# Kernel optimization log

Measured on AMD Instinct MI355X. Metric: run time of the kernel, lower is better.

## Reference

```python
import jax, jax.numpy as jnp
from jax import lax
import numpy as np

DN = ('NHWC', 'HWIO', 'NHWC')  # NHWC activations, HWIO kernels (TF layout)
EPS = 1e-3


def setup_inputs() -> dict:
    key = jax.random.key(0)
    ks = jax.random.split(key, 6)
    B, H, W, C = 16, 64, 64, 256
    x = jax.random.normal(ks[0], (B, H, W, C), jnp.float32)
    # per-sample predicted kernels (scaled to keep activations well-conditioned)
    depthwise_kernels = jax.random.normal(ks[1], (B, 3, 3, C, C), jnp.float32) * 0.02
    pointwise_kernels = jax.random.normal(ks[2], (B, 1, 1, C, C), jnp.float32) * 0.06
    biases = jax.random.normal(ks[3], (B, C), jnp.float32) * 0.1
    # shared trailing Conv2D layer params
    conv_w = jax.random.normal(ks[4], (3, 3, C, C), jnp.float32) * 0.02
    conv_b = jnp.zeros((C,), jnp.float32)
    return dict(x=x, depthwise_kernels=depthwise_kernels,
                pointwise_kernels=pointwise_kernels, biases=biases,
                conv_w=conv_w, conv_b=conv_b)


def _instance_norm(x):
    # tf.nn.moments over spatial dims (population variance), eps=0.001
    mean = jnp.mean(x, axis=(1, 2), keepdims=True)
    var = jnp.var(x, axis=(1, 2), keepdims=True)
    return (x - mean) * lax.rsqrt(var + EPS)


def _reflect_pad_hw(x, p=1):
    pad = [(0, 0)] * (x.ndim - 3) + [(p, p), (p, p), (0, 0)]
    return jnp.pad(x, pad, mode='reflect')


def _per_sample_conv(xi, dk, pk, bi):
    # xi: [H,W,C]; dk: [3,3,C,Cm]; pk: [1,1,Cm,Co]; bi: [Co]
    xp = _reflect_pad_hw(xi)[None]  # [1,H+2,W+2,C]
    y = lax.conv_general_dilated(xp, dk, (1, 1), 'VALID', dimension_numbers=DN)
    y = lax.conv_general_dilated(y, pk, (1, 1), 'VALID', dimension_numbers=DN)
    return (y + bi)[0]


def reference(x, depthwise_kernels, pointwise_kernels, biases, conv_w, conv_b):
    x = _instance_norm(x)
    # per-sample kernels -> vmap over batch (replaces tf.map_fn)
    x = jax.vmap(_per_sample_conv)(x, depthwise_kernels, pointwise_kernels, biases)
    # shared Conv2D: reflect pad + VALID conv + bias
    xp = _reflect_pad_hw(x)
    y = lax.conv_general_dilated(xp, conv_w, (1, 1), 'VALID', dimension_numbers=DN)
    return y + conv_b
```

## Files before the change

kernel.cpp:

```cpp
#include <hip/hip_runtime.h>


typedef __bf16 bf16x8 __attribute__((ext_vector_type(8)));
typedef float f32x4 __attribute__((ext_vector_type(4)));

__device__ __forceinline__ float bf2f(unsigned short v) {
    return __uint_as_float(((unsigned int)v) << 16);
}
__device__ __forceinline__ unsigned short f2bf(float f) {
    unsigned int u = __float_as_uint(f);
    unsigned int r = (u + 0x7FFFu + ((u >> 16) & 1u)) >> 16;
    return (unsigned short)r;
}
__device__ __forceinline__ float ldg_elem(const void* p, size_t idx, bool isbf) {
    return isbf ? bf2f(((const unsigned short*)p)[idx]) : ((const float*)p)[idx];
}

__device__ __forceinline__ void gload16(const void* g, void* l) {
    __builtin_amdgcn_global_load_lds(
        (__attribute__((address_space(1))) void*)(unsigned long long)g,
        (__attribute__((address_space(3))) void*)(unsigned long long)l,
        16, 0, 0);
}

#define RAW_BARRIER() do { asm volatile("" ::: "memory"); \
                           __builtin_amdgcn_s_barrier();   \
                           asm volatile("" ::: "memory"); } while (0)

__global__ void detect_dtype(const unsigned short* __restrict__ x, int* __restrict__ flag) {
    __shared__ int wild;
    if (threadIdx.x == 0) wild = 0;
    __syncthreads();
    int cnt = 0;
    for (int i = 0; i < 16; ++i) {
        float a = fabsf(bf2f(x[threadIdx.x * 16 + i]));
        if (!(a < 64.f) || (a != 0.f && a < 1e-5f)) cnt++;
    }
    atomicAdd(&wild, cnt);
    __syncthreads();
    if (threadIdx.x == 0) *flag = (wild > 512) ? 0 : 1;
}

__global__ void norm_partial2(const void* __restrict__ x, const int* __restrict__ flag,
                              float* __restrict__ partS, float* __restrict__ partQ) {
    const bool isbf = (*flag != 0);
    const int b = blockIdx.x, ch = blockIdx.y;
    const int t = threadIdx.x;
    const int l = t & 63;
    const int c4 = l * 4;
    const int sp0 = t >> 6;
    const size_t base = ((size_t)(b * 4096 + ch * 128 + sp0)) * 256 + c4;
    float s[4] = {0.f, 0.f, 0.f, 0.f}, q[4] = {0.f, 0.f, 0.f, 0.f};
    if (isbf) {
        for (int i = 0; i < 32; ++i) {
            const unsigned short* p = (const unsigned short*)x + base + (size_t)i * 1024;
            ushort4 v = *(const ushort4*)p;
            float a[4] = {bf2f(v.x), bf2f(v.y), bf2f(v.z), bf2f(v.w)};
#pragma unroll
            for (int j = 0; j < 4; ++j) { s[j] += a[j]; q[j] += a[j] * a[j]; }
        }
    } else {
        for (int i = 0; i < 32; ++i) {
            float4 v = *(const float4*)((const float*)x + base + (size_t)i * 1024);
            float a[4] = {v.x, v.y, v.z, v.w};
#pragma unroll
            for (int j = 0; j < 4; ++j) { s[j] += a[j]; q[j] += a[j] * a[j]; }
        }
    }
    __shared__ float red[4][64][9];
#pragma unroll
    for (int j = 0; j < 4; ++j) { red[sp0][l][j] = s[j]; red[sp0][l][4 + j] = q[j]; }
    __syncthreads();
    if (t < 64) {
#pragma unroll
        for (int j = 0; j < 4; ++j) {
            float ss = red[0][t][j] + red[1][t][j] + red[2][t][j] + red[3][t][j];
            float qq = red[0][t][4 + j] + red[1][t][4 + j] + red[2][t][4 + j] + red[3][t][4 + j];
            int c = t * 4 + j;
            partS[(b * 32 + ch) * 256 + c] = ss;
            partQ[(b * 32 + ch) * 256 + c] = qq;
        }
    }
}

__global__ void norm_finalize2(const float* __restrict__ partS, const float* __restrict__ partQ,
                               float* __restrict__ mean, float* __restrict__ rstd) {
    const int b = blockIdx.x, c = threadIdx.x;
    float s = 0.f, q = 0.f;
    for (int k = 0; k < 32; ++k) {
        s += partS[(b * 32 + k) * 256 + c];
        q += partQ[(b * 32 + k) * 256 + c];
    }
    float m = s * (1.f / 4096.f);
    float v = q * (1.f / 4096.f) - m * m;
    mean[b * 256 + c] = m;
    rstd[b * 256 + c] = rsqrtf(v + 1e-3f);
}

__global__ void norm_apply(const void* __restrict__ x, const int* __restrict__ flag,
                           const float* __restrict__ mean, const float* __restrict__ rstd,
                           unsigned short* __restrict__ xn) {
    const bool isbf = (*flag != 0);
    size_t e = ((size_t)blockIdx.x * 256 + threadIdx.x) * 8;
    int c0 = (int)(e & 255);
    int bc = (int)(e >> 20) * 256 + c0;
    float v[8];
    if (isbf) {
        uint4 raw = *(const uint4*)((const unsigned short*)x + e);
        unsigned int rr[4] = {raw.x, raw.y, raw.z, raw.w};
#pragma unroll
        for (int i = 0; i < 4; ++i) {
            v[2 * i]     = bf2f((unsigned short)(rr[i] & 0xFFFF));
            v[2 * i + 1] = bf2f((unsigned short)(rr[i] >> 16));
        }
    } else {
        float4 f0 = *(const float4*)((const float*)x + e);
        float4 f1 = *(const float4*)((const float*)x + e + 4);
        v[0] = f0.x; v[1] = f0.y; v[2] = f0.z; v[3] = f0.w;
        v[4] = f1.x; v[5] = f1.y; v[6] = f1.z; v[7] = f1.w;
    }
    unsigned int o[4];
#pragma unroll
    for (int i = 0; i < 4; ++i) {
        unsigned short lo = f2bf((v[2 * i]     - mean[bc + 2 * i])     * rstd[bc + 2 * i]);
        unsigned short hi = f2bf((v[2 * i + 1] - mean[bc + 2 * i + 1]) * rstd[bc + 2 * i + 1]);
        o[i] = (unsigned int)lo | ((unsigned int)hi << 16);
    }
    uint4 out; out.x = o[0]; out.y = o[1]; out.z = o[2]; out.w = o[3];
    *(uint4*)(xn + e) = out;
}

template <bool SCALE>
__global__ void transpose_wk(const void* __restrict__ src, const int* __restrict__ flag,
                             unsigned short* __restrict__ dst,
                             int s_per, long dstBStride, int coStride,
                             const float* __restrict__ rstd) {
    __shared__ unsigned short tile[64][66];
    const bool isbf = (*flag != 0);
    const int sl = blockIdx.x;
    const int b = sl / s_per;
    const size_t dbase = (size_t)b * (size_t)dstBStride + (size_t)(sl % s_per) * 256;
    const int ci0 = blockIdx.y * 64, co0 = blockIdx.z * 64;
    const int t = threadIdx.x;
    const int co4 = (t & 15) * 4;
    const int r0 = t >> 4;
#pragma unroll
    for (int i = 0; i < 4; ++i) {
        int r = r0 + i * 16;
        size_t sidx = (size_t)sl * 65536 + (size_t)(ci0 + r) * 256 + co0 + co4;
        if (isbf) {
            ushort4 v = *(const ushort4*)((const unsigned short*)src + sidx);
            tile[r][co4] = v.x; tile[r][co4 + 1] = v.y;
            tile[r][co4 + 2] = v.z; tile[r][co4 + 3] = v.w;
        } else {
            float4 v = *(const float4*)((const float*)src + sidx);
            tile[r][co4] = f2bf(v.x); tile[r][co4 + 1] = f2bf(v.y);
            tile[r][co4 + 2] = f2bf(v.z); tile[r][co4 + 3] = f2bf(v.w);
        }
    }
    __syncthreads();
    const int cip = (t & 31) * 2;
    const int cob = t >> 5;
    float s0 = 1.f, s1 = 1.f;
    if (SCALE) { s0 = rstd[b * 256 + ci0 + cip]; s1 = rstd[b * 256 + ci0 + cip + 1]; }
#pragma unroll
    for (int i = 0; i < 8; ++i) {
        int co = cob + i * 8;
        unsigned short lo = tile[cip][co], hi = tile[cip + 1][co];
        if (SCALE) { lo = f2bf(bf2f(lo) * s0); hi = f2bf(bf2f(hi) * s1); }
        *(unsigned int*)(dst + dbase + (size_t)(co0 + co) * coStride + ci0 + cip) =
            (unsigned int)lo | ((unsigned int)hi << 16);
    }
}

__global__ void corr_kernel(const unsigned short* __restrict__ dkT,
                            const float* __restrict__ mean,
                            float* __restrict__ negcorr) {
    const int b = blockIdx.x;
    const int lane = threadIdx.x & 63;
    const int co = blockIdx.y * 4 + (threadIdx.x >> 6);
    const unsigned short* wp = dkT + (size_t)(b * 256 + co) * 2304;
    const float* mb = mean + b * 256;
    const int ci0 = (lane & 31) * 8;
    float4 ma = *(const float4*)(mb + ci0);
    float4 mc = *(const float4*)(mb + ci0 + 4);
    float mm[8] = {ma.x, ma.y, ma.z, ma.w, mc.x, mc.y, mc.z, mc.w};
    float sum = 0.f;
#pragma unroll
    for (int c = 0; c < 5; ++c) {
        int k = c * 512 + lane * 8;
        if (k < 2304) {
            uint4 w = *(const uint4*)(wp + k);
            unsigned int wsv[4] = {w.x, w.y, w.z, w.w};
#pragma unroll
            for (int j = 0; j < 4; ++j) {
                sum += bf2f((unsigned short)(wsv[j] & 0xFFFF)) * mm[2 * j];
                sum += bf2f((unsigned short)(wsv[j] >> 16)) * mm[2 * j + 1];
            }
        }
    }
#pragma unroll
    for (int off = 32; off > 0; off >>= 1) sum += __shfl_down(sum, off);
    if (lane == 0) negcorr[b * 256 + co] = -sum;
}

template <bool PER_SAMPLE_W, int BIAS_MODE, bool OUT_F32>
__global__ __launch_bounds__(512, 2) void conv3x3_256(const unsigned short* __restrict__ src,
                                                      const int* __restrict__ flag,
                                                      const unsigned short* __restrict__ wT,
                                                      const void* __restrict__ bias,
                                                      void* __restrict__ dst) {
    constexpr int KTOT = 2304;
    extern __shared__ unsigned short smem[];

    const int t = threadIdx.x;
    const int lane = t & 63;
    const int wave = t >> 6;
    const int wr = wave >> 2;
    const int wc = wave & 3;
    const int bid = blockIdx.x + 16 * blockIdx.z;
    const int b  = (bid & 7) + ((bid >> 3) & 1) * 8;
    const int mt = bid >> 4;
    const int m0 = mt * 256;
    const int R0 = mt * 4;
    const unsigned short* srcB = src + (size_t)b * (4096 * 256);
    const unsigned short* wB = wT + (PER_SAMPLE_W ? (size_t)b * 256 * KTOT : (size_t)0);
    const bool in_bf = (BIAS_MODE >= 2) ? (*flag != 0) : true;

    const int wx = t >> 3;
    const int wg = ((t & 7) ^ (wx & 7)) << 3;
    int wrow[6];
#pragma unroll
    for (int u = 0; u < 6; ++u) {
        int r = R0 - 1 + u;
        wrow[u] = (r < 0) ? 1 : (r > 63 ? 62 : r);
    }
    const unsigned short* winsrc[6];
#pragma unroll
    for (int u = 0; u < 6; ++u)
        winsrc[u] = srcB + ((size_t)wrow[u] * 64 + wx) * 256 + wg;
    const unsigned short* bsrc = wB + (size_t)wx * KTOT + wg;

    f32x4 acc[8][4];
#pragma unroll
    for (int i = 0; i < 8; ++i)
#pragma unroll
        for (int j = 0; j < 4; ++j) acc[i][j] = (f32x4){0.f, 0.f, 0.f, 0.f};

    const int fr = lane & 15;
    const int quad = lane >> 4;
    const int fsw = fr & 7;
    const int ksb0 = (quad ^ fsw) << 3;
    const int ksb1 = ((quad + 4) ^ fsw) << 3;
    const int rm = wr * 128;
    const int cn = wc * 64;

#pragma unroll
    for (int u = 0; u < 6; ++u)
        gload16(winsrc[u], smem + u * 4096 + wave * 512);
#pragma unroll
    for (int u = 0; u < 4; ++u)
        gload16(bsrc + (size_t)u * 64 * KTOT, smem + 49152 + u * 4096 + wave * 512);

    bf16x8 af[4][2], bfr[4][2];

    for (int cg = 0; cg < 4; ++cg) {
        const unsigned short* winb = smem + (cg & 1) * 24576;
        for (int s = 0; s < 9; ++s) {
            const int j = cg * 9 + s;
            const int dh = s / 3 - 1;
            const int dw = s % 3 - 1;

            if (s == 6 || s == 7)      asm volatile("s_waitcnt vmcnt(2)" ::: "memory");
            else if (s == 8)           asm volatile("s_waitcnt vmcnt(1)" ::: "memory");
            else                       asm volatile("s_waitcnt vmcnt(0)" ::: "memory");
            RAW_BARRIER();

            if (j < 35) {
                const int s1 = (s == 8) ? 0 : s + 1;
                const int cg1 = (s == 8) ? cg + 1 : cg;
                const int koff1 = s1 * 256 + cg1 * 64;
                unsigned short* bdst = smem + 49152 + ((j + 1) & 1) * 16384 + wave * 512;
#pragma unroll
                for (int u = 0; u < 4; ++u)
                    gload16(bsrc + (size_t)u * 64 * KTOT + koff1, bdst + u * 4096);
            }
            if (cg < 3) {
                unsigned short* wdst = smem + ((cg + 1) & 1) * 24576 + wave * 512;
                const int cgo = (cg + 1) * 64;
                if (s == 5) {
                    gload16(winsrc[0] + cgo, wdst);
                    gload16(winsrc[1] + cgo, wdst + 4096);
                } else if (s == 6) {
                    gload16(winsrc[2] + cgo, wdst + 2 * 4096);
                    gload16(winsrc[3] + cgo, wdst + 3 * 4096);
                } else if (s == 7) {
                    gload16(winsrc[4] + cgo, wdst + 4 * 4096);
                } else if (s == 8) {
                    gload16(winsrc[5] + cgo, wdst + 5 * 4096);
                }
            }

            int aoo[4][2];
#pragma unroll
            for (int mi = 0; mi < 4; ++mi) {
                int ww = mi * 16 + fr + dw;
                ww = (ww < 0) ? 1 : (ww > 63 ? 62 : ww);
                const int x7 = ww & 7;
                aoo[mi][0] = ww * 64 + ((quad ^ x7) << 3);
                aoo[mi][1] = ww * 64 + (((quad + 4) ^ x7) << 3);
            }
            const unsigned short* A1 = winb + (wr * 2 + 1 + dh) * 4096;
            const unsigned short* A2 = A1 + 4096;
            const unsigned short* Bb = smem + 49152 + (j & 1) * 16384;

#pragma unroll
            for (int mi = 0; mi < 4; ++mi) {
                af[mi][0] = *(const bf16x8*)(A1 + aoo[mi][0]);
                af[mi][1] = *(const bf16x8*)(A1 + aoo[mi][1]);
            }
#pragma unroll
            for (int n = 0; n < 2; ++n) {
                const unsigned short* rp = Bb + (cn + n * 16 + fr) * 64;
                bfr[n][0] = *(const bf16x8*)(rp + ksb0);
                bfr[n][1] = *(const bf16x8*)(rp + ksb1);
            }
            __builtin_amdgcn_s_setprio(1);
#pragma unroll
            for (int mi = 0; mi < 4; ++mi)
#pragma unroll
                for (int n = 0; n < 2; ++n) {
                    acc[mi][n] = __builtin_amdgcn_mfma_f32_16x16x32_bf16(af[mi][0], bfr[n][0], acc[mi][n], 0, 0, 0);
                    acc[mi][n] = __builtin_amdgcn_mfma_f32_16x16x32_bf16(af[mi][1], bfr[n][1], acc[mi][n], 0, 0, 0);
                }
            __builtin_amdgcn_s_setprio(0);

#pragma unroll
            for (int n = 2; n < 4; ++n) {
                const unsigned short* rp = Bb + (cn + n * 16 + fr) * 64;
                bfr[n][0] = *(const bf16x8*)(rp + ksb0);
                bfr[n][1] = *(const bf16x8*)(rp + ksb1);
            }
            __builtin_amdgcn_s_setprio(1);
#pragma unroll
            for (int mi = 0; mi < 4; ++mi)
#pragma unroll
                for (int n = 2; n < 4; ++n) {
                    acc[mi][n] = __builtin_amdgcn_mfma_f32_16x16x32_bf16(af[mi][0], bfr[n][0], acc[mi][n], 0, 0, 0);
                    acc[mi][n] = __builtin_amdgcn_mfma_f32_16x16x32_bf16(af[mi][1], bfr[n][1], acc[mi][n], 0, 0, 0);
                }
            __builtin_amdgcn_s_setprio(0);

#pragma unroll
            for (int mi = 0; mi < 4; ++mi) {
                af[mi][0] = *(const bf16x8*)(A2 + aoo[mi][0]);
                af[mi][1] = *(const bf16x8*)(A2 + aoo[mi][1]);
            }
            __builtin_amdgcn_s_setprio(1);
#pragma unroll
            for (int mi = 0; mi < 4; ++mi)
#pragma unroll
                for (int n = 0; n < 4; ++n) {
                    acc[4 + mi][n] = __builtin_amdgcn_mfma_f32_16x16x32_bf16(af[mi][0], bfr[n][0], acc[4 + mi][n], 0, 0, 0);
                    acc[4 + mi][n] = __builtin_amdgcn_mfma_f32_16x16x32_bf16(af[mi][1], bfr[n][1], acc[4 + mi][n], 0, 0, 0);
                }
            __builtin_amdgcn_s_setprio(0);
        }
    }

    const int rbase = quad * 4;
    float bv[4];
#pragma unroll
    for (int n = 0; n < 4; ++n) {
        int nn = cn + n * 16 + fr;
        if (BIAS_MODE == 2)      bv[n] = ldg_elem(bias, b * 256 + nn, in_bf);
        else if (BIAS_MODE == 3) bv[n] = ldg_elem(bias, nn, in_bf);
        else                     bv[n] = 0.f;
    }
#pragma unroll
    for (int m = 0; m < 8; ++m) {
#pragma unroll
        for (int rr = 0; rr < 4; ++rr) {
            int mm = m0 + rm + m * 16 + rbase + rr;
            size_t rowoff = ((size_t)b * 4096 + mm) * 256;
#pragma unroll
            for (int n = 0; n < 4; ++n) {
                int nn = cn + n * 16 + fr;
                float val = acc[m][n][rr] + bv[n];
                if (OUT_F32) ((float*)dst)[rowoff + nn] = val;
                else         ((unsigned short*)dst)[rowoff + nn] = f2bf(val);
            }
        }
    }
}

template <int KSLICES, bool PER_SAMPLE_W, int BIAS_MODE, bool IS3X3, bool OUT_F32>
__global__ __launch_bounds__(512, 2) void gemm_conv_256(const unsigned short* __restrict__ src,
                                                        const int* __restrict__ flag,
                                                        const unsigned short* __restrict__ wT,
                                                        const void* __restrict__ bias,
                                                        void* __restrict__ dst) {
    constexpr int KTOT = KSLICES * 256;
    constexpr int NKT = KTOT / 64;
    static_assert(NKT >= 2, "pipeline needs >=2 K-tiles");
    extern __shared__ unsigned short smem[];

    const int t = threadIdx.x;
    const int lane = t & 63;
    const int wave = t >> 6;
    const int wr = wave >> 2;
    const int wc = wave & 3;
    const int bid = blockIdx.x + 16 * blockIdx.z;
    const int b  = (bid & 7) + ((bid >> 3) & 1) * 8;
    const int m0 = (bid >> 4) * 256;
    const unsigned short* srcB = src + (size_t)b * (4096 * 256);
    const unsigned short* wB = wT + (PER_SAMPLE_W ? (size_t)b * 256 * KTOT : (size_t)0);
    const bool in_bf = (BIAS_MODE >= 2) ? (*flag != 0) : true;

    const int trow = t >> 3;
    const int tswz = ((t & 7) ^ (trow & 7)) << 3;
    int hU[4], wU[4];
#pragma unroll
    for (int u = 0; u < 4; ++u) {
        int m = m0 + u * 64 + trow;
        hU[u] = m >> 6; wU[u] = m & 63;
    }
    const unsigned short* gBu[4];
#pragma unroll
    for (int u = 0; u < 4; ++u)
        gBu[u] = wB + (size_t)(u * 64 + trow) * KTOT + tswz;

    f32x4 acc[8][4];
#pragma unroll
    for (int i = 0; i < 8; ++i)
#pragma unroll
        for (int j = 0; j < 4; ++j) acc[i][j] = (f32x4){0.f, 0.f, 0.f, 0.f};

    const int fr = lane & 15;
    const int quad = lane >> 4;
    const int fsw = fr & 7;
    const int ks0 = ((quad) ^ fsw) << 3;
    const int ks1 = ((quad + 4) ^ fsw) << 3;
    const int rm = wr * 128;
    const int cn = wc * 64;

#pragma unroll
    for (int kt = 0; kt < 2; ++kt) {
        const int pdh = IS3X3 ? -1 : 0;
        const int pdw = IS3X3 ? -1 : 0;
        const int pchb = (kt & 3) << 6;
        unsigned short* ldsAW = smem + kt * 32768 + wave * 512;
#pragma unroll
        for (int u = 0; u < 4; ++u) {
            int hh = hU[u] + pdh; hh = (hh < 0) ? 1 : (hh > 63 ? 62 : hh);
            int ww = wU[u] + pdw; ww = (ww < 0) ? 1 : (ww > 63 ? 62 : ww);
            gload16(srcB + (size_t)((hh << 6) + ww) * 256 + pchb + tswz, ldsAW + u * 4096);
        }
#pragma unroll
        for (int u = 0; u < 4; ++u)
            gload16(gBu[u] + (size_t)kt * 64, ldsAW + 16384 + u * 4096);
    }
    asm volatile("s_waitcnt vmcnt(8)" ::: "memory");
    RAW_BARRIER();

    bf16x8 af[4][2], bfr[4][2];
    size_t aoff[4];
    int cur_s = -1;

    for (int i = 0; i < NKT; ++i) {
        const int buf = i & 1;
        const unsigned short* As_b = smem + buf * 32768;
        const unsigned short* Bs_b = As_b + 16384;
        unsigned short* ldsAW = smem + buf * 32768 + wave * 512;
        const int kt2 = i + 2;
        const bool st = (kt2 < NKT);

#pragma unroll
        for (int m = 0; m < 4; ++m) {
            const unsigned short* rp = As_b + (rm + m * 16 + fr) * 64;
            af[m][0] = *(const bf16x8*)(rp + ks0);
            af[m][1] = *(const bf16x8*)(rp + ks1);
        }
#pragma unroll
        for (int n = 0; n < 2; ++n) {
            const unsigned short* rp = Bs_b + (cn + n * 16 + fr) * 64;
            bfr[n][0] = *(const bf16x8*)(rp + ks0);
            bfr[n][1] = *(const bf16x8*)(rp + ks1);
        }
        __builtin_amdgcn_s_setprio(1);
#pragma unroll
        for (int m = 0; m < 4; ++m)
#pragma unroll
            for (int n = 0; n < 2; ++n) {
                acc[m][n] = __builtin_amdgcn_mfma_f32_16x16x32_bf16(af[m][0], bfr[n][0], acc[m][n], 0, 0, 0);
                acc[m][n] = __builtin_amdgcn_mfma_f32_16x16x32_bf16(af[m][1], bfr[n][1], acc[m][n], 0, 0, 0);
            }
        __builtin_amdgcn_s_setprio(0);

#pragma unroll
        for (int n = 2; n < 4; ++n) {
            const unsigned short* rp = Bs_b + (cn + n * 16 + fr) * 64;
            bfr[n][0] = *(const bf16x8*)(rp + ks0);
            bfr[n][1] = *(const bf16x8*)(rp + ks1);
        }
        __builtin_amdgcn_s_setprio(1);
#pragma unroll
        for (int m = 0; m < 4; ++m)
#pragma unroll
            for (int n = 2; n < 4; ++n) {
                acc[m][n] = __builtin_amdgcn_mfma_f32_16x16x32_bf16(af[m][0], bfr[n][0], acc[m][n], 0, 0, 0);
                acc[m][n] = __builtin_amdgcn_mfma_f32_16x16x32_bf16(af[m][1], bfr[n][1], acc[m][n], 0, 0, 0);
            }
        __builtin_amdgcn_s_setprio(0);

#pragma unroll
        for (int m = 0; m < 4; ++m) {
            const unsigned short* rp = As_b + (rm + 64 + m * 16 + fr) * 64;
            af[m][0] = *(const bf16x8*)(rp + ks0);
            af[m][1] = *(const bf16x8*)(rp + ks1);
        }
        __builtin_amdgcn_s_setprio(1);
#pragma unroll
        for (int m = 0; m < 4; ++m)
#pragma unroll
            for (int n = 0; n < 4; ++n) {
                acc[4 + m][n] = __builtin_amdgcn_mfma_f32_16x16x32_bf16(af[m][0], bfr[n][0], acc[4 + m][n], 0, 0, 0);
                acc[4 + m][n] = __builtin_amdgcn_mfma_f32_16x16x32_bf16(af[m][1], bfr[n][1], acc[4 + m][n], 0, 0, 0);
            }
        __builtin_amdgcn_s_setprio(0);

        RAW_BARRIER();
        if (st) {
            if (IS3X3) {
                const int s2 = kt2 >> 2;
                if (s2 != cur_s) {
                    cur_s = s2;
                    const int dh2 = s2 / 3 - 1, dw2 = s2 % 3 - 1;
#pragma unroll
                    for (int u = 0; u < 4; ++u) {
                        int hh = hU[u] + dh2; hh = (hh < 0) ? 1 : (hh > 63 ? 62 : hh);
                        int ww = wU[u] + dw2; ww = (ww < 0) ? 1 : (ww > 63 ? 62 : ww);
                        aoff[u] = (size_t)((hh << 6) + ww) * 256 + tswz;
                    }
                }
            } else if (cur_s < 0) {
                cur_s = 0;
#pragma unroll
                for (int u = 0; u < 4; ++u)
                    aoff[u] = (size_t)((hU[u] << 6) + wU[u]) * 256 + tswz;
            }
            const int chb2 = (kt2 & 3) << 6;
#pragma unroll
            for (int u = 0; u < 4; ++u)
                gload16(srcB + aoff[u] + chb2, ldsAW + u * 4096);
#pragma unroll
            for (int u = 0; u < 4; ++u)
                gload16(gBu[u] + (size_t)kt2 * 64, ldsAW + 16384 + u * 4096);
            asm volatile("s_waitcnt vmcnt(8)" ::: "memory");
        } else if (i + 1 < NKT) {
            asm volatile("s_waitcnt vmcnt(0)" ::: "memory");
        }
        RAW_BARRIER();
    }

    const int rbase = quad * 4;
    float bv[4];
#pragma unroll
    for (int n = 0; n < 4; ++n) {
        int nn = cn + n * 16 + fr;
        if (BIAS_MODE == 2)      bv[n] = ldg_elem(bias, b * 256 + nn, in_bf);
        else if (BIAS_MODE == 3) bv[n] = ldg_elem(bias, nn, in_bf);
        else                     bv[n] = 0.f;
    }
#pragma unroll
    for (int m = 0; m < 8; ++m) {
#pragma unroll
        for (int rr = 0; rr < 4; ++rr) {
            int mm = m0 + rm + m * 16 + rbase + rr;
            size_t rowoff = ((size_t)b * 4096 + mm) * 256;
#pragma unroll
            for (int n = 0; n < 4; ++n) {
                int nn = cn + n * 16 + fr;
                float val = acc[m][n][rr] + bv[n];
                if (OUT_F32) ((float*)dst)[rowoff + nn] = val;
                else         ((unsigned short*)dst)[rowoff + nn] = f2bf(val);
            }
        }
    }
}

template <int KSLICES, bool PER_SAMPLE_W, int BIAS_MODE, bool IS3X3, bool SRC_ADAPT, bool OUT_F32>
__global__ __launch_bounds__(256) void gemm_conv(const void* __restrict__ src,
                                                 const int* __restrict__ flag,
                                                 const unsigned short* __restrict__ wT,
                                                 const void* __restrict__ bias,
                                                 void* __restrict__ dst) {
    constexpr int KTOT = KSLICES * 256;
    __shared__ unsigned short As[128][40];
    __shared__ unsigned short Bs[128][40];

    const bool in_bf = (SRC_ADAPT || BIAS_MODE >= 2) ? (*flag != 0) : true;
    const int t = threadIdx.x;
    const int b = blockIdx.z;
    const int m0 = blockIdx.x * 128;
    const int n0 = blockIdx.y * 128;
    const size_t srcOfs = (size_t)b * (4096 * 256);
    const unsigned short* wB = wT + (PER_SAMPLE_W ? (size_t)b * 256 * KTOT : (size_t)0);

    f32x4 acc[4][4];
#pragma unroll
    for (int i = 0; i < 4; ++i)
#pragma unroll
        for (int j = 0; j < 4; ++j) acc[i][j] = (f32x4){0.f, 0.f, 0.f, 0.f};

    const int lane = t & 63;
    const int wave = t >> 6;
    const int rm = (wave >> 1) * 64;
    const int cn = (wave & 1) * 64;
    const int fr = lane & 15;
    const int kg = (lane >> 4) * 8;

    for (int kk = 0; kk < KTOT / 32; ++kk) {
        const int k0 = kk * 32;
        const int s = k0 >> 8;
        const int ci0 = k0 & 255;
        const int dh = IS3X3 ? (s / 3) - 1 : 0;
        const int dw = IS3X3 ? (s % 3) - 1 : 0;
        __syncthreads();
#pragma unroll
        for (int cc = 0; cc < 2; ++cc) {
            int ch = t + cc * 256;
            int r = ch >> 2;
            int ko = (ch & 3) << 3;
            int m = m0 + r;
            int h = m >> 6, w = m & 63;
            if (IS3X3) {
                h += dh; h = (h < 0) ? 1 : (h > 63 ? 62 : h);
                w += dw; w = (w < 0) ? 1 : (w > 63 ? 62 : w);
            }
            size_t eidx = srcOfs + (size_t)((h << 6) + w) * 256 + ci0 + ko;
            if (!SRC_ADAPT || in_bf) {
                uint4 v = *(const uint4*)((const unsigned short*)src + eidx);
                *(uint4*)&As[r][ko] = v;
            } else {
                const float* sf = (const float*)src + eidx;
                float4 f0 = *(const float4*)sf;
                float4 f1 = *(const float4*)(sf + 4);
                uint4 v;
                v.x = (unsigned int)f2bf(f0.x) | ((unsigned int)f2bf(f0.y) << 16);
                v.y = (unsigned int)f2bf(f0.z) | ((unsigned int)f2bf(f0.w) << 16);
                v.z = (unsigned int)f2bf(f1.x) | ((unsigned int)f2bf(f1.y) << 16);
                v.w = (unsigned int)f2bf(f1.z) | ((unsigned int)f2bf(f1.w) << 16);
                *(uint4*)&As[r][ko] = v;
            }
        }
#pragma unroll
        for (int cc = 0; cc < 2; ++cc) {
            int ch = t + cc * 256;
            int n = ch >> 2;
            int ko = (ch & 3) << 3;
            uint4 v = *(const uint4*)(wB + (size_t)(n0 + n) * KTOT + k0 + ko);
            *(uint4*)&Bs[n][ko] = v;
        }
        __syncthreads();

        bf16x8 af[4], bfr[4];
#pragma unroll
        for (int i = 0; i < 4; ++i) af[i] = *(const bf16x8*)&As[rm + i * 16 + fr][kg];
#pragma unroll
        for (int j = 0; j < 4; ++j) bfr[j] = *(const bf16x8*)&Bs[cn + j * 16 + fr][kg];
#pragma unroll
        for (int i = 0; i < 4; ++i)
#pragma unroll
            for (int j = 0; j < 4; ++j)
                acc[i][j] = __builtin_amdgcn_mfma_f32_16x16x32_bf16(af[i], bfr[j], acc[i][j], 0, 0, 0);
    }

    const int rbase = (lane >> 4) * 4;
    const int col = lane & 15;
    float bv[4];
#pragma unroll
    for (int j = 0; j < 4; ++j) {
        int n = n0 + cn + j * 16 + col;
        if (BIAS_MODE == 1)      bv[j] = ((const float*)bias)[b * 256 + n];
        else if (BIAS_MODE == 2) bv[j] = ldg_elem(bias, b * 256 + n, in_bf);
        else if (BIAS_MODE == 3) bv[j] = ldg_elem(bias, n, in_bf);
        else                     bv[j] = 0.f;
    }
#pragma unroll
    for (int i = 0; i < 4; ++i) {
#pragma unroll
        for (int rr = 0; rr < 4; ++rr) {
            int m = m0 + rm + i * 16 + rbase + rr;
            size_t rowoff = ((size_t)b * 4096 + m) * 256;
#pragma unroll
            for (int j = 0; j < 4; ++j) {
                int n = n0 + cn + j * 16 + col;
                float val = acc[i][j][rr] + bv[j];
                if (OUT_F32) ((float*)dst)[rowoff + n] = val;
                else         ((unsigned short*)dst)[rowoff + n] = f2bf(val);
            }
        }
    }
}

extern "C" void kernel_launch(void* const* d_in, const int* in_sizes, int n_in,
                              void* d_out, int out_size, void* d_ws, size_t ws_size,
                              hipStream_t stream) {
    const void* x    = d_in[0];
    const void* dk   = d_in[1];
    const void* pk   = d_in[2];
    const void* bias = d_in[3];
    const void* cw   = d_in[4];
    const void* cb   = d_in[5];

    const size_t NEED_SMALL = 36896768u;
    const size_t NEED_BIG   = 55771136u;
    if (ws_size < NEED_SMALL) return;
    const bool big = (ws_size >= NEED_BIG);

    char* ws = (char*)d_ws;
    int*   flagp   = (int*)ws;
    float* meanp   = (float*)(ws + 1024);
    float* rstdp   = (float*)(ws + 17408);
    float* negcorr = (float*)(ws + 33792);
    unsigned short* pkT = (unsigned short*)(ws + 65536);
    unsigned short* cwT = (unsigned short*)(ws + 2162688);
    unsigned short* dkT = (unsigned short*)(ws + 3342336);
    unsigned short* xn  = (unsigned short*)(ws + 22216704);
    float* partS = (float*)(ws + 22216704);
    float* partQ = (float*)(ws + 22216704 + 524288);
    unsigned short* y2  = big ? xn : dkT;
    unsigned short* y1  = (unsigned short*)d_out;

    hipFuncSetAttribute(reinterpret_cast<const void*>(conv3x3_256<true, 0, false>),
                        hipFuncAttributeMaxDynamicSharedMemorySize, 163840);
    hipFuncSetAttribute(reinterpret_cast<const void*>(conv3x3_256<false, 3, true>),
                        hipFuncAttributeMaxDynamicSharedMemorySize, 163840);
    hipFuncSetAttribute(reinterpret_cast<const void*>(gemm_conv_256<1, true, 2, false, false>),
                        hipFuncAttributeMaxDynamicSharedMemorySize, 131072);

    detect_dtype<<<1, 256, 0, stream>>>((const unsigned short*)x, flagp);
    norm_partial2<<<dim3(16, 32), 256, 0, stream>>>(x, flagp, partS, partQ);
    norm_finalize2<<<16, 256, 0, stream>>>(partS, partQ, meanp, rstdp);

    transpose_wk<false><<<dim3(16, 4, 4), 256, 0, stream>>>(pk, flagp, pkT, 1, 65536L, 256, nullptr);
    transpose_wk<false><<<dim3(9, 4, 4), 256, 0, stream>>>(cw, flagp, cwT, 9, 0L, 2304, nullptr);

    if (big) {
        transpose_wk<false><<<dim3(144, 4, 4), 256, 0, stream>>>(dk, flagp, dkT, 9, 589824L, 2304, nullptr);
        norm_apply<<<8192, 256, 0, stream>>>(x, flagp, meanp, rstdp, xn);
        conv3x3_256<true, 0, false><<<dim3(16, 1, 16), 512, 163840, stream>>>(xn, flagp, dkT, nullptr, y1);
    } else {
        transpose_wk<true><<<dim3(144, 4, 4), 256, 0, stream>>>(dk, flagp, dkT, 9, 589824L, 2304, rstdp);
        corr_kernel<<<dim3(16, 64), 256, 0, stream>>>(dkT, meanp, negcorr);
        gemm_conv<9, true, 1, true, true, false><<<dim3(32, 2, 16), 256, 0, stream>>>(x, flagp, dkT, negcorr, y1);
    }

    gemm_conv_256<1, true, 2, false, false><<<dim3(16, 1, 16), 512, 131072, stream>>>(y1, flagp, pkT, bias, y2);
    conv3x3_256<false, 3, true><<<dim3(16, 1, 16), 512, 163840, stream>>>(y2, flagp, cwT, cb, d_out);
}
```

Before: 332.0 us.

## Restructure conv3x3 pipeline: single input window buffer, triple-buffered weight tiles

Changes the conv3x3_256 load pipeline from double-buffered input windows with double-buffered weight tiles to one input window buffer and a 3-deep ring of weight tiles, issued two steps ahead. The next channel group's window is now reloaded synchronously at each group boundary, behind an extra wait and barrier, instead of being prefetched during the previous group. Dynamic shared memory drops from 163840 to 147456 bytes. The aim is a deeper weight prefetch and a smaller LDS footprint, at the cost of exposed window-reload latency four times per block.

```diff
diff --git a/kernel.cpp b/kernel.cpp
--- a/kernel.cpp
+++ b/kernel.cpp
@@ -241,6 +241,15 @@
         winsrc[u] = srcB + ((size_t)wrow[u] * 64 + wx) * 256 + wg;
     const unsigned short* bsrc = wB + (size_t)wx * KTOT + wg;
 
+    auto issueB = [&](int jn) {
+        const int sn = jn % 9, cgn = jn / 9;
+        const int koff = sn * 256 + cgn * 64;
+        unsigned short* bdst = smem + 24576 + (jn % 3) * 16384 + wave * 512;
+#pragma unroll
+        for (int u = 0; u < 4; ++u)
+            gload16(bsrc + (size_t)u * 64 * KTOT + koff, bdst + u * 4096);
+    };
+
     f32x4 acc[8][4];
 #pragma unroll
     for (int i = 0; i < 8; ++i)
@@ -258,47 +267,36 @@
 #pragma unroll
     for (int u = 0; u < 6; ++u)
         gload16(winsrc[u], smem + u * 4096 + wave * 512);
-#pragma unroll
-    for (int u = 0; u < 4; ++u)
-        gload16(bsrc + (size_t)u * 64 * KTOT, smem + 49152 + u * 4096 + wave * 512);
+    issueB(0);
+    issueB(1);
 
     bf16x8 af[4][2], bfr[4][2];
 
     for (int cg = 0; cg < 4; ++cg) {
-        const unsigned short* winb = smem + (cg & 1) * 24576;
         for (int s = 0; s < 9; ++s) {
             const int j = cg * 9 + s;
             const int dh = s / 3 - 1;
             const int dw = s % 3 - 1;
 
-            if (s == 6 || s == 7)      asm volatile("s_waitcnt vmcnt(2)" ::: "memory");
-            else if (s == 8)           asm volatile("s_waitcnt vmcnt(1)" ::: "memory");
-            else                       asm volatile("s_waitcnt vmcnt(0)" ::: "memory");
-            RAW_BARRIER();
-
-            if (j < 35) {
-                const int s1 = (s == 8) ? 0 : s + 1;
-                const int cg1 = (s == 8) ? cg + 1 : cg;
-                const int koff1 = s1 * 256 + cg1 * 64;
-                unsigned short* bdst = smem + 49152 + ((j + 1) & 1) * 16384 + wave * 512;
-#pragma unroll
-                for (int u = 0; u < 4; ++u)
-                    gload16(bsrc + (size_t)u * 64 * KTOT + koff1, bdst + u * 4096);
-            }
-            if (cg < 3) {
-                unsigned short* wdst = smem + ((cg + 1) & 1) * 24576 + wave * 512;
-                const int cgo = (cg + 1) * 64;
-                if (s == 5) {
-                    gload16(winsrc[0] + cgo, wdst);
-                    gload16(winsrc[1] + cgo, wdst + 4096);
-                } else if (s == 6) {
-                    gload16(winsrc[2] + cgo, wdst + 2 * 4096);
-                    gload16(winsrc[3] + cgo, wdst + 3 * 4096);
-                } else if (s == 7) {
-                    gload16(winsrc[4] + cgo, wdst + 4 * 4096);
-                } else if (s == 8) {
-                    gload16(winsrc[5] + cgo, wdst + 5 * 4096);
+            if (s == 0) {
+                asm volatile("s_waitcnt vmcnt(4)" ::: "memory");
+                RAW_BARRIER();
+                if (cg > 0) {
+                    const int cgo = cg * 64;
+#pragma unroll
+                    for (int u = 0; u < 6; ++u)
+                        gload16(winsrc[u] + cgo, smem + u * 4096 + wave * 512);
+                    issueB(j + 2);
+                    asm volatile("s_waitcnt vmcnt(4)" ::: "memory");
+                    RAW_BARRIER();
+                } else {
+                    issueB(j + 2);
                 }
+            } else {
+                if (j < 35) asm volatile("s_waitcnt vmcnt(4)" ::: "memory");
+                else        asm volatile("s_waitcnt vmcnt(0)" ::: "memory");
+                RAW_BARRIER();
+                if (j + 2 <= 35) issueB(j + 2);
             }
 
             int aoo[4][2];
@@ -310,9 +308,9 @@
                 aoo[mi][0] = ww * 64 + ((quad ^ x7) << 3);
                 aoo[mi][1] = ww * 64 + (((quad + 4) ^ x7) << 3);
             }
-            const unsigned short* A1 = winb + (wr * 2 + 1 + dh) * 4096;
+            const unsigned short* A1 = smem + (wr * 2 + 1 + dh) * 4096;
             const unsigned short* A2 = A1 + 4096;
-            const unsigned short* Bb = smem + 49152 + (j & 1) * 16384;
+            const unsigned short* Bb = smem + 24576 + (s % 3) * 16384;
 
 #pragma unroll
             for (int mi = 0; mi < 4; ++mi) {
@@ -734,9 +732,9 @@
     unsigned short* y1  = (unsigned short*)d_out;
 
     hipFuncSetAttribute(reinterpret_cast<const void*>(conv3x3_256<true, 0, false>),
-                        hipFuncAttributeMaxDynamicSharedMemorySize, 163840);
+                        hipFuncAttributeMaxDynamicSharedMemorySize, 147456);
     hipFuncSetAttribute(reinterpret_cast<const void*>(conv3x3_256<false, 3, true>),
-                        hipFuncAttributeMaxDynamicSharedMemorySize, 163840);
+                        hipFuncAttributeMaxDynamicSharedMemorySize, 147456);
     hipFuncSetAttribute(reinterpret_cast<const void*>(gemm_conv_256<1, true, 2, false, false>),
                         hipFuncAttributeMaxDynamicSharedMemorySize, 131072);
 
@@ -750,7 +748,7 @@
     if (big) {
         transpose_wk<false><<<dim3(144, 4, 4), 256, 0, stream>>>(dk, flagp, dkT, 9, 589824L, 2304, nullptr);
         norm_apply<<<8192, 256, 0, stream>>>(x, flagp, meanp, rstdp, xn);
-        conv3x3_256<true, 0, false><<<dim3(16, 1, 16), 512, 163840, stream>>>(xn, flagp, dkT, nullptr, y1);
+        conv3x3_256<true, 0, false><<<dim3(16, 1, 16), 512, 147456, stream>>>(xn, flagp, dkT, nullptr, y1);
     } else {
         transpose_wk<true><<<dim3(144, 4, 4), 256, 0, stream>>>(dk, flagp, dkT, 9, 589824L, 2304, rstdp);
         corr_kernel<<<dim3(16, 64), 256, 0, stream>>>(dkT, meanp, negcorr);
@@ -758,5 +756,5 @@
     }
 
     gemm_conv_256<1, true, 2, false, false><<<dim3(16, 1, 16), 512, 131072, stream>>>(y1, flagp, pkT, bias, y2);
-    conv3x3_256<false, 3, true><<<dim3(16, 1, 16), 512, 163840, stream>>>(y2, flagp, cwT, cb, d_out);
-}
+    conv3x3_256<false, 3, true><<<dim3(16, 1, 16), 512, 147456, stream>>>(y2, flagp, cwT, cb, d_out);
+}
```

Result: no change. 336.8 us (+1.4%).

## Retile 3x3 conv waves to 4x2 layout with prefetched A fragments

Applied to the files above, without the earlier changes.

Changes the wave layout of the 3x3 conv kernel from 2x4 (128 rows x 64 cols per wave) to 4x2 (64 rows x 128 cols per wave), so each wave handles one image row and all eight N fragments. A fragments for the next tap are prefetched from LDS after the current MFMAs, which hides LDS latency behind compute. The vmcnt wait logic is adjusted for the last channel group. In exchange, B-operand LDS traffic per wave doubles while A traffic halves, and prefetching A keeps more fragments live in registers.

```diff
diff --git a/kernel.cpp b/kernel.cpp
--- a/kernel.cpp
+++ b/kernel.cpp
@@ -216,8 +216,8 @@
     const int t = threadIdx.x;
     const int lane = t & 63;
     const int wave = t >> 6;
-    const int wr = wave >> 2;
-    const int wc = wave & 3;
+    const int wr = wave >> 1;
+    const int wc = wave & 1;
     const int bid = blockIdx.x + 16 * blockIdx.z;
     const int b  = (bid & 7) + ((bid >> 3) & 1) * 8;
     const int mt = bid >> 4;
@@ -241,28 +241,34 @@
         winsrc[u] = srcB + ((size_t)wrow[u] * 64 + wx) * 256 + wg;
     const unsigned short* bsrc = wB + (size_t)wx * KTOT + wg;
 
-    f32x4 acc[8][4];
-#pragma unroll
-    for (int i = 0; i < 8; ++i)
-#pragma unroll
-        for (int j = 0; j < 4; ++j) acc[i][j] = (f32x4){0.f, 0.f, 0.f, 0.f};
+    auto issueB = [&](int jn) {
+        const int sn = jn % 9, cgn = jn / 9;
+        const int koff = sn * 256 + cgn * 64;
+        unsigned short* bdst = smem + 49152 + (jn & 1) * 16384 + wave * 512;
+#pragma unroll
+        for (int u = 0; u < 4; ++u)
+            gload16(bsrc + (size_t)u * 64 * KTOT + koff, bdst + u * 4096);
+    };
+
+    f32x4 acc[4][8];
+#pragma unroll
+    for (int i = 0; i < 4; ++i)
+#pragma unroll
+        for (int j = 0; j < 8; ++j) acc[i][j] = (f32x4){0.f, 0.f, 0.f, 0.f};
 
     const int fr = lane & 15;
     const int quad = lane >> 4;
     const int fsw = fr & 7;
     const int ksb0 = (quad ^ fsw) << 3;
     const int ksb1 = ((quad + 4) ^ fsw) << 3;
-    const int rm = wr * 128;
-    const int cn = wc * 64;
+    const int cn = wc * 128;
 
 #pragma unroll
     for (int u = 0; u < 6; ++u)
         gload16(winsrc[u], smem + u * 4096 + wave * 512);
-#pragma unroll
-    for (int u = 0; u < 4; ++u)
-        gload16(bsrc + (size_t)u * 64 * KTOT, smem + 49152 + u * 4096 + wave * 512);
-
-    bf16x8 af[4][2], bfr[4][2];
+    issueB(0);
+
+    bf16x8 afp[4][2], bfr[4][2];
 
     for (int cg = 0; cg < 4; ++cg) {
         const unsigned short* winb = smem + (cg & 1) * 24576;
@@ -271,20 +277,13 @@
             const int dh = s / 3 - 1;
             const int dw = s % 3 - 1;
 
-            if (s == 6 || s == 7)      asm volatile("s_waitcnt vmcnt(2)" ::: "memory");
-            else if (s == 8)           asm volatile("s_waitcnt vmcnt(1)" ::: "memory");
-            else                       asm volatile("s_waitcnt vmcnt(0)" ::: "memory");
+            const int keep = (cg < 3) ? ((s == 6 || s == 7) ? 2 : (s == 8 ? 1 : 0)) : 0;
+            if (keep == 2)      asm volatile("s_waitcnt vmcnt(2)" ::: "memory");
+            else if (keep == 1) asm volatile("s_waitcnt vmcnt(1)" ::: "memory");
+            else                asm volatile("s_waitcnt vmcnt(0)" ::: "memory");
             RAW_BARRIER();
 
-            if (j < 35) {
-                const int s1 = (s == 8) ? 0 : s + 1;
-                const int cg1 = (s == 8) ? cg + 1 : cg;
-                const int koff1 = s1 * 256 + cg1 * 64;
-                unsigned short* bdst = smem + 49152 + ((j + 1) & 1) * 16384 + wave * 512;
-#pragma unroll
-                for (int u = 0; u < 4; ++u)
-                    gload16(bsrc + (size_t)u * 64 * KTOT + koff1, bdst + u * 4096);
-            }
+            if (j < 35) issueB(j + 1);
             if (cg < 3) {
                 unsigned short* wdst = smem + ((cg + 1) & 1) * 24576 + wave * 512;
                 const int cgo = (cg + 1) * 64;
@@ -301,90 +300,87 @@
                 }
             }
 
-            int aoo[4][2];
-#pragma unroll
-            for (int mi = 0; mi < 4; ++mi) {
-                int ww = mi * 16 + fr + dw;
-                ww = (ww < 0) ? 1 : (ww > 63 ? 62 : ww);
-                const int x7 = ww & 7;
-                aoo[mi][0] = ww * 64 + ((quad ^ x7) << 3);
-                aoo[mi][1] = ww * 64 + (((quad + 4) ^ x7) << 3);
-            }
-            const unsigned short* A1 = winb + (wr * 2 + 1 + dh) * 4096;
-            const unsigned short* A2 = A1 + 4096;
             const unsigned short* Bb = smem + 49152 + (j & 1) * 16384;
 
 #pragma unroll
-            for (int mi = 0; mi < 4; ++mi) {
-                af[mi][0] = *(const bf16x8*)(A1 + aoo[mi][0]);
-                af[mi][1] = *(const bf16x8*)(A1 + aoo[mi][1]);
-            }
-#pragma unroll
-            for (int n = 0; n < 2; ++n) {
+            for (int n = 0; n < 4; ++n) {
                 const unsigned short* rp = Bb + (cn + n * 16 + fr) * 64;
                 bfr[n][0] = *(const bf16x8*)(rp + ksb0);
                 bfr[n][1] = *(const bf16x8*)(rp + ksb1);
             }
+            if (s == 0) {
+                const unsigned short* A1 = winb + (wr + 1 + dh) * 4096;
+#pragma unroll
+                for (int mi = 0; mi < 4; ++mi) {
+                    int ww = mi * 16 + fr + dw;
+                    ww = (ww < 0) ? 1 : (ww > 63 ? 62 : ww);
+                    const int x7 = ww & 7;
+                    afp[mi][0] = *(const bf16x8*)(A1 + ww * 64 + ((quad ^ x7) << 3));
+                    afp[mi][1] = *(const bf16x8*)(A1 + ww * 64 + (((quad + 4) ^ x7) << 3));
+                }
+            }
+
             __builtin_amdgcn_s_setprio(1);
 #pragma unroll
             for (int mi = 0; mi < 4; ++mi)
 #pragma unroll
-                for (int n = 0; n < 2; ++n) {
-                    acc[mi][n] = __builtin_amdgcn_mfma_f32_16x16x32_bf16(af[mi][0], bfr[n][0], acc[mi][n], 0, 0, 0);
-                    acc[mi][n] = __builtin_amdgcn_mfma_f32_16x16x32_bf16(af[mi][1], bfr[n][1], acc[mi][n], 0, 0, 0);
+                for (int n = 0; n < 4; ++n) {
+                    acc[mi][n] = __builtin_amdgcn_mfma_f32_16x16x32_bf16(afp[mi][0], bfr[n][0], acc[mi][n], 0, 0, 0);
+                    acc[mi][n] = __builtin_amdgcn_mfma_f32_16x16x32_bf16(afp[mi][1], bfr[n][1], acc[mi][n], 0, 0, 0);
                 }
             __builtin_amdgcn_s_setprio(0);
 
 #pragma unroll
-            for (int n = 2; n < 4; ++n) {
-                const unsigned short* rp = Bb + (cn + n * 16 + fr) * 64;
+            for (int n = 0; n < 4; ++n) {
+                const unsigned short* rp = Bb + (cn + (n + 4) * 16 + fr) * 64;
                 bfr[n][0] = *(const bf16x8*)(rp + ksb0);
                 bfr[n][1] = *(const bf16x8*)(rp + ksb1);
             }
+
             __builtin_amdgcn_s_setprio(1);
 #pragma unroll
             for (int mi = 0; mi < 4; ++mi)
 #pragma unroll
-                for (int n = 2; n < 4; ++n) {
-                    acc[mi][n] = __builtin_amdgcn_mfma_f32_16x16x32_bf16(af[mi][0], bfr[n][0], acc[mi][n], 0, 0, 0);
-                    acc[mi][n] = __builtin_amdgcn_mfma_f32_16x16x32_bf16(af[mi][1], bfr[n][1], acc[mi][n], 0, 0, 0);
+                for (int n = 0; n < 4; ++n) {
+                    acc[mi][n + 4] = __builtin_amdgcn_mfma_f32_16x16x32_bf16(afp[mi][0], bfr[n][0], acc[mi][n + 4], 0, 0, 0);
+                    acc[mi][n + 4] = __builtin_amdgcn_mfma_f32_16x16x32_bf16(afp[mi][1], bfr[n][1], acc[mi][n + 4], 0, 0, 0);
                 }
             __builtin_amdgcn_s_setprio(0);
 
-#pragma unroll
-            for (int mi = 0; mi < 4; ++mi) {
-                af[mi][0] = *(const bf16x8*)(A2 + aoo[mi][0]);
-                af[mi][1] = *(const bf16x8*)(A2 + aoo[mi][1]);
-            }
-            __builtin_amdgcn_s_setprio(1);
-#pragma unroll
-            for (int mi = 0; mi < 4; ++mi)
-#pragma unroll
-                for (int n = 0; n < 4; ++n) {
-                    acc[4 + mi][n] = __builtin_amdgcn_mfma_f32_16x16x32_bf16(af[mi][0], bfr[n][0], acc[4 + mi][n], 0, 0, 0);
-                    acc[4 + mi][n] = __builtin_amdgcn_mfma_f32_16x16x32_bf16(af[mi][1], bfr[n][1], acc[4 + mi][n], 0, 0, 0);
+            if (s < 8) {
+                const int s1 = s + 1;
+                const int dh1 = s1 / 3 - 1;
+                const int dw1 = s1 % 3 - 1;
+                const unsigned short* A1n = winb + (wr + 1 + dh1) * 4096;
+#pragma unroll
+                for (int mi = 0; mi < 4; ++mi) {
+                    int ww = mi * 16 + fr + dw1;
+                    ww = (ww < 0) ? 1 : (ww > 63 ? 62 : ww);
+                    const int x7 = ww & 7;
+                    afp[mi][0] = *(const bf16x8*)(A1n + ww * 64 + ((quad ^ x7) << 3));
+                    afp[mi][1] = *(const bf16x8*)(A1n + ww * 64 + (((quad + 4) ^ x7) << 3));
                 }
-            __builtin_amdgcn_s_setprio(0);
+            }
         }
     }
 
     const int rbase = quad * 4;
-    float bv[4];
-#pragma unroll
-    for (int n = 0; n < 4; ++n) {
+    float bv[8];
+#pragma unroll
+    for (int n = 0; n < 8; ++n) {
         int nn = cn + n * 16 + fr;
         if (BIAS_MODE == 2)      bv[n] = ldg_elem(bias, b * 256 + nn, in_bf);
         else if (BIAS_MODE == 3) bv[n] = ldg_elem(bias, nn, in_bf);
         else                     bv[n] = 0.f;
     }
 #pragma unroll
-    for (int m = 0; m < 8; ++m) {
+    for (int m = 0; m < 4; ++m) {
 #pragma unroll
         for (int rr = 0; rr < 4; ++rr) {
-            int mm = m0 + rm + m * 16 + rbase + rr;
+            int mm = m0 + wr * 64 + m * 16 + rbase + rr;
             size_t rowoff = ((size_t)b * 4096 + mm) * 256;
 #pragma unroll
-            for (int n = 0; n < 4; ++n) {
+            for (int n = 0; n < 8; ++n) {
                 int nn = cn + n * 16 + fr;
                 float val = acc[m][n][rr] + bv[n];
                 if (OUT_F32) ((float*)dst)[rowoff + nn] = val;
```

Result: no change. 335.0 us (+0.9%).
